# Kernel optimization log

Measured on AMD Instinct MI355X. Metric: run time of the kernel, lower is better.

## Reference

```python
import jax, jax.numpy as jnp
import numpy as np

T, N, C = 1024, 4, 4
RADIUS, COMPRESSION = 256, 1
TAU = 2.0  # LIF filter time constant (LIF_Filter source unavailable; exponential leaky integrator assumed)


def _build_delay():
    # Mirrors JeffressFilter.__init__ delay construction exactly.
    neg = np.arange(-RADIUS, 0, COMPRESSION, dtype=np.int64)
    pos = np.arange(RADIUS, 0, -COMPRESSION, dtype=np.int64)[::-1]
    _d = np.concatenate([neg, pos]).reshape(-1, 1)            # (D_out, 1)
    delay = np.maximum(np.concatenate([_d, -_d], axis=1), 0)  # relu -> (D_out, 2)
    return jnp.asarray(delay, dtype=jnp.int32)


def setup_inputs() -> dict:
    key = jax.random.key(0)
    k1, k2 = jax.random.split(key)
    x = jax.random.normal(k1, (T, N, C, 2), dtype=jnp.float32)
    delay = _build_delay()                                   # (D_out, 2) int
    d_out = delay.shape[0]                                   # 512
    # get_weight(1.0, 10.0, compression) source unavailable; stand-in float vector per output channel
    weight = jax.random.normal(k2, (d_out,), dtype=jnp.float32)
    return {"x": x, "weight": weight, "delay": delay}


def _lif_filter(x):
    # Leaky integrator over time axis 0: v[t] = exp(-1/tau) * v[t-1] + x[t]
    decay = jnp.asarray(np.exp(-1.0 / TAU), dtype=x.dtype)

    def step(v, xt):
        v = decay * v + xt
        return v, v

    _, y = jax.lax.scan(step, jnp.zeros(x.shape[1:], x.dtype), x)
    return y  # (T, N, C, 2)


def reference(x, weight, delay):
    Tlen = x.shape[0]
    y = _lif_filter(x)                                       # (T, N, C, 2)

    t = jnp.arange(Tlen, dtype=jnp.int32)
    # SpikeDelay.forward: mask rows t >= T - delay to 0, then gather at (t - delay) % T.
    # Equivalent post-gather: out[t] = y[t - delay] if t >= delay else 0 (zero-padded shift).
    t_idx = (t[:, None, None] - delay[None]) % Tlen          # (T, D_out, 2)
    i_idx = jnp.arange(2, dtype=jnp.int32)[None, None, :]    # broadcast over (T, D_out, 2)
    yt = jnp.moveaxis(y, -1, 1)                              # (T, 2, N, C)
    gathered = yt[t_idx, i_idx]                              # (T, D_out, 2, N, C)
    mask = t[:, None, None] >= delay[None]                   # (T, D_out, 2)
    out = jnp.where(mask[..., None, None], gathered, 0.0)
    out = out.sum(axis=2)                                    # sum over in_features=2 -> (T, D_out, N, C)
    out = jnp.moveaxis(out, 1, -1)                           # (T, N, C, D_out)
    return out * weight                                      # scale per output channel
```

## Files before the change

### kernel.cpp

```cpp
#include <hip/hip_runtime.h>


#define T_LEN  1024
#define D_OUT  512
#define NC     16
#define PAD    256
#define ROW    (PAD + T_LEN)
#define YB_OFF (NC * ROW)

__global__ __launch_bounds__(64) void lif_scan_kernel(const float* __restrict__ x,
                                                      float* __restrict__ ws) {
    const int tid = threadIdx.x;
    const int b   = blockIdx.x;

    #pragma unroll
    for (int k = 0; k < 8; ++k) {
        const int id = (b * 64 + tid) * 8 + k;
        const int r  = id >> 8;
        const int c  = id & 255;
        ws[r * ROW + c] = 0.0f;
    }

    if (tid < 32) {
        const int ch = tid;
        const int nc = ch >> 1;
        const int i  = ch & 1;
        float* row = ws + (i ? YB_OFF : 0) + nc * ROW + PAD;

        const int   t0    = b * 64;
        const float decay = 0.60653065971263342f;

        float v = 0.0f;
        #pragma unroll 8
        for (int k = 0; k < 64; ++k) {
            const int t = t0 - 64 + k;
            const float xv = (t >= 0) ? x[t * 32 + ch] : 0.0f;
            v = decay * v + xv;
        }
        #pragma unroll 8
        for (int k = 0; k < 64; ++k) {
            const int t = t0 + k;
            v = decay * v + x[t * 32 + ch];
            row[t] = v;
        }
    }
}

__global__ __launch_bounds__(256) void jeffress_kernel(const float* __restrict__ ws,
                                                       const float* __restrict__ w,
                                                       const int* __restrict__ delay,
                                                       float4* __restrict__ out) {
    const int bid = blockIdx.x;
    const int nc  = bid & 15;
    const int t0  = (bid >> 4) * 16 + (threadIdx.x >> 7) * 8;
    const int d4  = threadIdx.x & 127;
    const int d   = d4 * 4;

    const int4*   dp  = (const int4*)(delay + 2 * d);
    const int4    e01 = dp[0];
    const int4    e23 = dp[1];
    const float4  wv  = ((const float4*)w)[d4];

    const float* A = ws + nc * ROW + PAD + t0;
    const float* B = ws + YB_OFF + nc * ROW + PAD + t0;
    const float* a0 = A - e01.x;  const float* b0 = B - e01.y;
    const float* a1 = A - e01.z;  const float* b1 = B - e01.w;
    const float* a2 = A - e23.x;  const float* b2 = B - e23.y;
    const float* a3 = A - e23.z;  const float* b3 = B - e23.w;

    float4* op = out + (size_t)t0 * (NC * D_OUT / 4) + nc * (D_OUT / 4) + d4;

    #pragma unroll
    for (int j = 0; j < 8; ++j) {
        float4 o;
        o.x = wv.x * (a0[j] + b0[j]);
        o.y = wv.y * (a1[j] + b1[j]);
        o.z = wv.z * (a2[j] + b2[j]);
        o.w = wv.w * (a3[j] + b3[j]);
        op[j * (NC * D_OUT / 4)] = o;
    }
}

extern "C" void kernel_launch(void* const* d_in, const int* in_sizes, int n_in,
                              void* d_out, int out_size, void* d_ws, size_t ws_size,
                              hipStream_t stream) {
    const float* x      = (const float*)d_in[0];
    const float* weight = (const float*)d_in[1];
    const int*   delay  = (const int*)d_in[2];
    float* out = (float*)d_out;
    float* ws  = (float*)d_ws;

    lif_scan_kernel<<<16, 64, 0, stream>>>(x, ws);

    const int nblocks = (T_LEN / 16) * NC;
    jeffress_kernel<<<nblocks, 256, 0, stream>>>(ws, weight, delay, (float4*)out);
}
```

Baseline: 79.13 us.

## Split LIF scan into finer chunks and remap Jeffress kernel to scalar per-lane stores

```diff
diff --git a/kernel.cpp b/kernel.cpp
--- a/kernel.cpp
+++ b/kernel.cpp
@@ -14,70 +14,57 @@
     const int b   = blockIdx.x;
 
     #pragma unroll
-    for (int k = 0; k < 8; ++k) {
-        const int id = (b * 64 + tid) * 8 + k;
+    for (int k = 0; k < 4; ++k) {
+        const int id = (b * 64 + tid) * 4 + k;
         const int r  = id >> 8;
         const int c  = id & 255;
         ws[r * ROW + c] = 0.0f;
     }
 
-    if (tid < 32) {
-        const int ch = tid;
-        const int nc = ch >> 1;
-        const int i  = ch & 1;
-        float* row = ws + (i ? YB_OFF : 0) + nc * ROW + PAD;
+    const int ch    = tid & 31;
+    const int chunk = b * 2 + (tid >> 5);
+    const int nc    = ch >> 1;
+    const int i     = ch & 1;
+    float* row = ws + (i ? YB_OFF : 0) + nc * ROW + PAD;
 
-        const int   t0    = b * 64;
-        const float decay = 0.60653065971263342f;
+    const int   t0    = chunk * 16;
+    const float decay = 0.60653065971263342f;
 
-        float v = 0.0f;
-        #pragma unroll 8
-        for (int k = 0; k < 64; ++k) {
-            const int t = t0 - 64 + k;
-            const float xv = (t >= 0) ? x[t * 32 + ch] : 0.0f;
-            v = decay * v + xv;
-        }
-        #pragma unroll 8
-        for (int k = 0; k < 64; ++k) {
-            const int t = t0 + k;
-            v = decay * v + x[t * 32 + ch];
-            row[t] = v;
-        }
+    float v = 0.0f;
+    #pragma unroll 16
+    for (int k = 0; k < 64; ++k) {
+        const int t = t0 - 64 + k;
+        const float xv = (t >= 0) ? x[t * 32 + ch] : 0.0f;
+        v = decay * v + xv;
+    }
+    #pragma unroll
+    for (int k = 0; k < 16; ++k) {
+        const int t = t0 + k;
+        v = decay * v + x[t * 32 + ch];
+        row[t] = v;
     }
 }
 
 __global__ __launch_bounds__(256) void jeffress_kernel(const float* __restrict__ ws,
                                                        const float* __restrict__ w,
-                                                       const int* __restrict__ delay,
-                                                       float4* __restrict__ out) {
-    const int bid = blockIdx.x;
-    const int nc  = bid & 15;
-    const int t0  = (bid >> 4) * 16 + (threadIdx.x >> 7) * 8;
-    const int d4  = threadIdx.x & 127;
-    const int d   = d4 * 4;
+                                                       const int2* __restrict__ delay,
+                                                       float* __restrict__ out) {
+    const int wid  = blockIdx.x * 4 + (threadIdx.x >> 6);
+    const int lane = threadIdx.x & 63;
+    const int t    = wid >> 4;
+    const int nc   = wid & 15;
 
-    const int4*   dp  = (const int4*)(delay + 2 * d);
-    const int4    e01 = dp[0];
-    const int4    e23 = dp[1];
-    const float4  wv  = ((const float4*)w)[d4];
-
-    const float* A = ws + nc * ROW + PAD + t0;
-    const float* B = ws + YB_OFF + nc * ROW + PAD + t0;
-    const float* a0 = A - e01.x;  const float* b0 = B - e01.y;
-    const float* a1 = A - e01.z;  const float* b1 = B - e01.w;
-    const float* a2 = A - e23.x;  const float* b2 = B - e23.y;
-    const float* a3 = A - e23.z;  const float* b3 = B - e23.w;
-
-    float4* op = out + (size_t)t0 * (NC * D_OUT / 4) + nc * (D_OUT / 4) + d4;
+    const float* A = ws + nc * ROW + PAD;
+    const float* B = A + YB_OFF;
+    float* orow = out + ((size_t)(t * NC + nc)) * D_OUT;
 
     #pragma unroll
-    for (int j = 0; j < 8; ++j) {
-        float4 o;
-        o.x = wv.x * (a0[j] + b0[j]);
-        o.y = wv.y * (a1[j] + b1[j]);
-        o.z = wv.z * (a2[j] + b2[j]);
-        o.w = wv.w * (a3[j] + b3[j]);
-        op[j * (NC * D_OUT / 4)] = o;
+    for (int g = 0; g < 8; ++g) {
+        const int d  = g * 64 + lane;
+        const int2 e = delay[d];
+        const float u0 = A[t - e.x];
+        const float u1 = B[t - e.y];
+        orow[d] = w[d] * (u0 + u1);
     }
 }
 
@@ -90,8 +77,8 @@
     float* out = (float*)d_out;
     float* ws  = (float*)d_ws;
 
-    lif_scan_kernel<<<16, 64, 0, stream>>>(x, ws);
+    lif_scan_kernel<<<32, 64, 0, stream>>>(x, ws);
 
-    const int nblocks = (T_LEN / 16) * NC;
-    jeffress_kernel<<<nblocks, 256, 0, stream>>>(ws, weight, delay, (float4*)out);
+    jeffress_kernel<<<(T_LEN * NC) / 4, 256, 0, stream>>>(
+        ws, weight, (const int2*)delay, (float4*)out ? (float*)out : (float*)out);
 }
```

Measured after the change: 78.32 us. About the same (-1.0%).
